# Optimization experiments

Measured on AMD Instinct MI355X. Metric: run time of the kernel, lower is better.

## Reference

```python
import jax, jax.numpy as jnp
import numpy as np

B = 512
NODES_PER_GRAPH = 256
N = B * NODES_PER_GRAPH
IN_DIM = 128
HID = 128
PAD_VALUE = -10000.0


def setup_inputs() -> dict:
    key = jax.random.key(0)
    ks = jax.random.split(key, 10)
    inp = {
        "last_node_batch": jax.random.normal(ks[0], (B, IN_DIM), jnp.float32),
        "h": jax.random.normal(ks[1], (N, HID), jnp.float32),
        # NodeEmbed: Linear(in_dim, hidden_dim)
        "W_embed": jax.random.normal(ks[2], (IN_DIM, HID), jnp.float32) / np.sqrt(IN_DIM),
        "b_embed": jnp.zeros((HID,), jnp.float32),
        # Linear_3(2H, 2H, 2)
        "W1": jax.random.normal(ks[3], (2 * HID, 2 * HID), jnp.float32) / np.sqrt(2 * HID),
        "b1": jnp.zeros((2 * HID,), jnp.float32),
        "W2": jax.random.normal(ks[4], (2 * HID, 2 * HID), jnp.float32) / np.sqrt(2 * HID),
        "b2": jnp.zeros((2 * HID,), jnp.float32),
        "W3": jax.random.normal(ks[5], (2 * HID, 2), jnp.float32) / np.sqrt(2 * HID),
        "b3": jnp.zeros((2,), jnp.float32),
        # ragged batch encoded as sorted segment ids (graph id per node)
        "segment_ids": jnp.repeat(jnp.arange(B, dtype=jnp.int64), NODES_PER_GRAPH),
        "max_nodes": NODES_PER_GRAPH,
    }
    return inp


def reference(last_node_batch, h, W_embed, b_embed, W1, b1, W2, b2, W3, b3,
              segment_ids, max_nodes):
    n = h.shape[0]
    b = last_node_batch.shape[0]
    # per-graph node embed, broadcast to each node of its graph (repeat+cat loop)
    node_embed = last_node_batch @ W_embed + b_embed          # [B, H]
    bcast = node_embed[segment_ids]                           # [N, H]
    stack = jnp.concatenate([h, bcast], axis=1)               # [N, 2H]
    # Linear_3 MLP
    out = jnp.tanh(stack @ W1 + b1)
    out = jnp.tanh(out @ W2 + b2)
    edges = out @ W3 + b3                                     # [N, 2]
    # unbatch + pad_sequence(padding_value=-10000), then flatten(1, -1)
    counts = jax.ops.segment_sum(jnp.ones((n,), jnp.int32), segment_ids, num_segments=b)
    offsets = jnp.cumsum(counts) - counts                     # start index of each graph
    pos = jnp.arange(n) - offsets[segment_ids]                # position within graph
    padded = jnp.full((b, max_nodes, 2), PAD_VALUE, dtype=edges.dtype)
    padded = padded.at[segment_ids, pos].set(edges)
    return padded.reshape(b, max_nodes * 2)
```

## Files before the change

kernel.cpp:

```cpp
#include <hip/hip_runtime.h>


typedef __attribute__((ext_vector_type(8))) short s16x8;
typedef __attribute__((ext_vector_type(4))) float f32x4;

#define K2   256
#define KH   128
#define LDK  264

__device__ __forceinline__ float b2f(unsigned short u) {
  return __builtin_bit_cast(float, (unsigned int)u << 16);
}
__device__ __forceinline__ unsigned short f2b(float f) {
  unsigned int u = __builtin_bit_cast(unsigned int, f);
  u += 0x7fffu + ((u >> 16) & 1u);
  return (unsigned short)(u >> 16);
}
__device__ __forceinline__ float pade_tanh(float x) {
  float x2 = x * x;
  float x4 = x2 * x2;
  float num = x * (945.0f + 105.0f * x2 + x4);
  float den = __builtin_fmaf(15.0f, x4, __builtin_fmaf(420.0f, x2, 945.0f));
  float r = num * __builtin_amdgcn_rcpf(den);
  return __builtin_fmaxf(-1.0f, __builtin_fminf(1.0f, r));
}
__device__ __forceinline__ unsigned int probe_is16(const unsigned int* wraw,
                                                   int t) {
  unsigned int w = wraw[t];
  unsigned int e = (w >> 7) & 0xFFu;
  unsigned long long m = __ballot(e >= 96 && e < 128);
  return (__popcll(m) >= 32) ? 1u : 0u;
}

__global__ __launch_bounds__(256) void prep_pack(
    const void* __restrict__ W1, const void* __restrict__ W2,
    const void* __restrict__ Wemb,
    unsigned short* __restrict__ W1P, unsigned short* __restrict__ W2P)
{
  __shared__ unsigned int flagLds;
  const int blk = blockIdx.x, t = threadIdx.x;
  if (t < 64) { unsigned int f = probe_is16((const unsigned int*)Wemb, t);
                if (t == 0) flagLds = f; }
  __syncthreads();
  const bool is16 = flagLds != 0u;

  const void* S; unsigned short* D; int k0, n0, pk;
  if (blk < 32) { S = W1; D = W1P; pk = 2048;
                  k0 = (blk & 3) * 32; n0 = (blk >> 2) * 32; }
  else { int b = blk - 32; S = W2; D = W2P; pk = 4096;
         k0 = (b & 7) * 32; n0 = (b >> 3) * 32; }
  #pragma unroll
  for (int q = 0; q < 4; ++q) {
    int idx = t + 256 * q;
    int ln = idx & 31, lk = idx >> 5;
    int n = n0 + ln, k = k0 + lk;
    unsigned short v = is16
        ? ((const unsigned short*)S)[k * K2 + n]
        : f2b(((const float*)S)[k * K2 + n]);
    D[(n >> 4) * pk + (k >> 3) * 128 + (n & 15) * 8 + (k & 7)] = v;
  }
}

__global__ __launch_bounds__(256, 3) void mlp_graph(
    const void* __restrict__ h,     const void* __restrict__ last,
    const void* __restrict__ Wemb,  const void* __restrict__ bemb,
    const void* __restrict__ W1,    const void* __restrict__ b1,
    const void* __restrict__ b2,
    const void* __restrict__ W3,    const void* __restrict__ b3,
    const unsigned short* __restrict__ W1P,
    const unsigned short* __restrict__ W2P,
    void* __restrict__ out)
{
  __shared__ __align__(16) unsigned short smA[32 * LDK];
  __shared__ float embp[2][KH];
  __shared__ float emb32[KH];
  __shared__ float ebias[K2];
  __shared__ float headp[4][32][2];
  __shared__ unsigned int flagLds;

  const int t    = threadIdx.x;
  const int lane = t & 63, w = t >> 6;
  const int quad = lane >> 4, l16 = lane & 15;
  const int g    = blockIdx.x >> 2;
  const int sp   = blockIdx.x & 3;

  if (t < 64) { unsigned int f = probe_is16((const unsigned int*)Wemb, t);
                if (t == 0) flagLds = f; }
  __syncthreads();
  const bool is16 = flagLds != 0u;

  {
    const int j = t & 127, half = t >> 7, k0 = half * 64;
    float a0 = 0.f, a1 = 0.f, a2 = 0.f, a3 = 0.f;
    if (is16) {
      const unsigned short* lp = (const unsigned short*)last + g * KH;
      const unsigned short* wp = (const unsigned short*)Wemb;
      #pragma unroll 4
      for (int k = k0; k < k0 + 64; k += 4) {
        a0 += b2f(lp[k])     * b2f(wp[k * KH + j]);
        a1 += b2f(lp[k + 1]) * b2f(wp[(k + 1) * KH + j]);
        a2 += b2f(lp[k + 2]) * b2f(wp[(k + 2) * KH + j]);
        a3 += b2f(lp[k + 3]) * b2f(wp[(k + 3) * KH + j]);
      }
    } else {
      const float* lp = (const float*)last + g * KH;
      const float* wp = (const float*)Wemb;
      #pragma unroll 4
      for (int k = k0; k < k0 + 64; k += 4) {
        a0 += lp[k]     * wp[k * KH + j];
        a1 += lp[k + 1] * wp[(k + 1) * KH + j];
        a2 += lp[k + 2] * wp[(k + 2) * KH + j];
        a3 += lp[k + 3] * wp[(k + 3) * KH + j];
      }
    }
    embp[half][j] = (a0 + a1) + (a2 + a3);
  }

  s16x8 bh[2];
  #pragma unroll
  for (int s = 0; s < 2; ++s) {
    int kk = 2 * w + s;
    #pragma unroll
    for (int j = 0; j < 8; ++j) {
      int kidx = (kk * 32 + quad * 8 + j) * 2 + (l16 & 1);
      bh[s][j] = is16 ? (short)((const unsigned short*)W3)[kidx]
                      : (short)f2b(((const float*)W3)[kidx]);
    }
  }
  float b2v[4];
  #pragma unroll
  for (int c = 0; c < 4; ++c) {
    int col = w * 64 + c * 16 + l16;
    b2v[c] = is16 ? b2f(((const unsigned short*)b2)[col])
                  : ((const float*)b2)[col];
  }
  float b3e = 0.f;
  if (t < 64)
    b3e = is16 ? b2f(((const unsigned short*)b3)[t & 1])
               : ((const float*)b3)[t & 1];
  __syncthreads();

  if (t < KH) {
    float e = is16 ? b2f(((const unsigned short*)bemb)[t])
                   : ((const float*)bemb)[t];
    emb32[t] = e + embp[0][t] + embp[1][t];
  }
  __syncthreads();

  {
    float s = is16 ? b2f(((const unsigned short*)b1)[t])
                   : ((const float*)b1)[t];
    if (is16) {
      const unsigned short* wp = (const unsigned short*)W1
                                 + (size_t)KH * K2 + t;
      #pragma unroll 4
      for (int k = 0; k < KH; ++k)
        s = __builtin_fmaf(emb32[k], b2f(wp[(size_t)k * K2]), s);
    } else {
      const float* wp = (const float*)W1 + (size_t)KH * K2 + t;
      #pragma unroll 4
      for (int k = 0; k < KH; ++k)
        s = __builtin_fmaf(emb32[k], wp[(size_t)k * K2], s);
    }
    ebias[t] = s;
  }

  uint4 hreg[2];
  const int pr = t >> 4, pc = t & 15;
  auto load_tile = [&](int slice) {
    int rbase = g * 256 + slice * 32;
    if (is16) {
      const uint4* hp = (const uint4*)h;
      #pragma unroll
      for (int i = 0; i < 2; ++i)
        hreg[i] = hp[(size_t)(rbase + pr + 16 * i) * 16 + pc];
    } else {
      const float4* hf = (const float4*)h;
      #pragma unroll
      for (int i = 0; i < 2; ++i) {
        float4 va = hf[(size_t)(rbase + pr + 16 * i) * 32 + pc * 2];
        float4 vb = hf[(size_t)(rbase + pr + 16 * i) * 32 + pc * 2 + 1];
        ushort4 ua, ub;
        ua.x = f2b(va.x); ua.y = f2b(va.y); ua.z = f2b(va.z); ua.w = f2b(va.w);
        ub.x = f2b(vb.x); ub.y = f2b(vb.y); ub.z = f2b(vb.z); ub.w = f2b(vb.w);
        hreg[i] = make_uint4(
            (unsigned)ua.x | ((unsigned)ua.y << 16),
            (unsigned)ua.z | ((unsigned)ua.w << 16),
            (unsigned)ub.x | ((unsigned)ub.y << 16),
            (unsigned)ub.z | ((unsigned)ub.w << 16));
      }
    }
  };
  load_tile(2 * sp);

  f32x4 acc[2][4];
  for (int tt = 0; tt < 2; ++tt) {
    const int slice = 2 * sp + tt;
    const int base = g * 256 + slice * 32;
    __syncthreads();
    #pragma unroll
    for (int i = 0; i < 2; ++i)
      *(uint4*)&smA[(pr + 16 * i) * LDK + pc * 8] = hreg[i];
    if (tt < 1) load_tile(slice + 1);
    __syncthreads();

    #pragma unroll
    for (int i = 0; i < 2; ++i)
      #pragma unroll
      for (int c = 0; c < 4; ++c) acc[i][c] = f32x4{0.f, 0.f, 0.f, 0.f};
    #pragma unroll
    for (int kk = 0; kk < 4; ++kk) {
      s16x8 a[2], b[4];
      #pragma unroll
      for (int i = 0; i < 2; ++i)
        a[i] = *(const s16x8*)&smA[(i * 16 + l16) * LDK + kk * 32 + quad * 8];
      #pragma unroll
      for (int c = 0; c < 4; ++c)
        b[c] = *(const s16x8*)&W1P[(w * 4 + c) * 2048
                                   + (kk * 4 + quad) * 128 + l16 * 8];
      #pragma unroll
      for (int i = 0; i < 2; ++i)
        #pragma unroll
        for (int c = 0; c < 4; ++c)
          acc[i][c] = __builtin_amdgcn_mfma_f32_16x16x32_bf16(
              a[i], b[c], acc[i][c], 0, 0, 0);
    }
    __syncthreads();
    #pragma unroll
    for (int c = 0; c < 4; ++c) {
      int col = w * 64 + c * 16 + l16;
      float eb = ebias[col];
      #pragma unroll
      for (int i = 0; i < 2; ++i)
        #pragma unroll
        for (int rg = 0; rg < 4; ++rg)
          smA[(i * 16 + quad * 4 + rg) * LDK + col] =
              f2b(pade_tanh(acc[i][c][rg] + eb));
    }
    __syncthreads();

    #pragma unroll
    for (int i = 0; i < 2; ++i)
      #pragma unroll
      for (int c = 0; c < 4; ++c) acc[i][c] = f32x4{0.f, 0.f, 0.f, 0.f};
    #pragma unroll 2
    for (int kk = 0; kk < 8; ++kk) {
      s16x8 a[2], b[4];
      #pragma unroll
      for (int i = 0; i < 2; ++i)
        a[i] = *(const s16x8*)&smA[(i * 16 + l16) * LDK + kk * 32 + quad * 8];
      #pragma unroll
      for (int c = 0; c < 4; ++c)
        b[c] = *(const s16x8*)&W2P[(w * 4 + c) * 4096
                                   + (kk * 4 + quad) * 128 + l16 * 8];
      #pragma unroll
      for (int i = 0; i < 2; ++i)
        #pragma unroll
        for (int c = 0; c < 4; ++c)
          acc[i][c] = __builtin_amdgcn_mfma_f32_16x16x32_bf16(
              a[i], b[c], acc[i][c], 0, 0, 0);
    }
    __syncthreads();
    #pragma unroll
    for (int c = 0; c < 4; ++c) {
      int col = w * 64 + c * 16 + l16;
      #pragma unroll
      for (int i = 0; i < 2; ++i)
        #pragma unroll
        for (int rg = 0; rg < 4; ++rg)
          smA[(i * 16 + quad * 4 + rg) * LDK + col] =
              f2b(pade_tanh(acc[i][c][rg] + b2v[c]));
    }
    __syncthreads();

    {
      #pragma unroll
      for (int i = 0; i < 2; ++i) acc[i][0] = f32x4{0.f, 0.f, 0.f, 0.f};
      #pragma unroll
      for (int s = 0; s < 2; ++s) {
        int kk = 2 * w + s;
        #pragma unroll
        for (int i = 0; i < 2; ++i) {
          s16x8 a = *(const s16x8*)&smA[(i * 16 + l16) * LDK
                                        + kk * 32 + quad * 8];
          acc[i][0] = __builtin_amdgcn_mfma_f32_16x16x32_bf16(
              a, bh[s], acc[i][0], 0, 0, 0);
        }
      }
      if (l16 < 2) {
        #pragma unroll
        for (int i = 0; i < 2; ++i)
          #pragma unroll
          for (int rg = 0; rg < 4; ++rg)
            headp[w][i * 16 + quad * 4 + rg][l16] = acc[i][0][rg];
      }
    }
    __syncthreads();
    if (t < 64) {
      const int r = t >> 1, e = t & 1;
      float s = b3e + headp[0][r][e] + headp[1][r][e]
                    + headp[2][r][e] + headp[3][r][e];
      size_t idx = (size_t)(base + r) * 2 + e;
      if (is16) ((unsigned short*)out)[idx] = f2b(s);
      else      ((float*)out)[idx] = s;
    }
  }
}

extern "C" void kernel_launch(void* const* d_in, const int* in_sizes, int n_in,
                              void* d_out, int out_size, void* d_ws, size_t ws_size,
                              hipStream_t stream) {
  (void)in_sizes; (void)n_in; (void)out_size; (void)ws_size;
  const void* last = d_in[0];
  const void* h    = d_in[1];
  const void* Wemb = d_in[2];
  const void* bemb = d_in[3];
  const void* W1   = d_in[4];
  const void* b1   = d_in[5];
  const void* W2   = d_in[6];
  const void* b2   = d_in[7];
  const void* W3   = d_in[8];
  const void* b3   = d_in[9];

  char* ws = (char*)d_ws;
  unsigned short* W1P   = (unsigned short*)(ws);
  unsigned short* W2P   = (unsigned short*)(ws + 65536);

  prep_pack<<<dim3(96), dim3(256), 0, stream>>>(W1, W2, Wemb, W1P, W2P);
  mlp_graph<<<dim3(2048), dim3(256), 0, stream>>>(
      h, last, Wemb, bemb, W1, b1, b2, W3, b3, W1P, W2P, d_out);
}
```

Measured before the change: 186.6 us.

## Use one 512-thread block per graph instead of four 256-thread blocks

The grid drops from four blocks per graph to one 512-thread block per graph, which walks four 64-row tiles. The eight waves split into four column groups and two row halves. This removes the per-graph prologue that was repeated four times (node embed, ebias matvec over W1, W3 fragments). In exchange there are only 512 blocks, which gives less parallelism and a longer serial loop per block, and LDS use per block doubles.

Measured after the change: 191.6 us. +2.7%, slower.

```diff
diff --git a/kernel.cpp b/kernel.cpp
--- a/kernel.cpp
+++ b/kernel.cpp
@@ -61,7 +61,7 @@
   }
 }
 
-__global__ __launch_bounds__(256, 3) void mlp_graph(
+__global__ __launch_bounds__(512, 2) void mlp_graph(
     const void* __restrict__ h,     const void* __restrict__ last,
     const void* __restrict__ Wemb,  const void* __restrict__ bemb,
     const void* __restrict__ W1,    const void* __restrict__ b1,
@@ -71,18 +71,19 @@
     const unsigned short* __restrict__ W2P,
     void* __restrict__ out)
 {
-  __shared__ __align__(16) unsigned short smA[32 * LDK];
-  __shared__ float embp[2][KH];
+  __shared__ __align__(16) unsigned short smA[64 * LDK];
+  __shared__ float embp[4][KH];
   __shared__ float emb32[KH];
   __shared__ float ebias[K2];
-  __shared__ float headp[4][32][2];
+  __shared__ float headp[4][64][2];
   __shared__ unsigned int flagLds;
 
   const int t    = threadIdx.x;
   const int lane = t & 63, w = t >> 6;
+  const int wc   = w & 3;
+  const int wrh  = w >> 2;
   const int quad = lane >> 4, l16 = lane & 15;
-  const int g    = blockIdx.x >> 2;
-  const int sp   = blockIdx.x & 3;
+  const int g    = blockIdx.x;
 
   if (t < 64) { unsigned int f = probe_is16((const unsigned int*)Wemb, t);
                 if (t == 0) flagLds = f; }
@@ -90,13 +91,13 @@
   const bool is16 = flagLds != 0u;
 
   {
-    const int j = t & 127, half = t >> 7, k0 = half * 64;
+    const int j = t & 127, qtr = t >> 7, k0 = qtr * 32;
     float a0 = 0.f, a1 = 0.f, a2 = 0.f, a3 = 0.f;
     if (is16) {
       const unsigned short* lp = (const unsigned short*)last + g * KH;
       const unsigned short* wp = (const unsigned short*)Wemb;
       #pragma unroll 4
-      for (int k = k0; k < k0 + 64; k += 4) {
+      for (int k = k0; k < k0 + 32; k += 4) {
         a0 += b2f(lp[k])     * b2f(wp[k * KH + j]);
         a1 += b2f(lp[k + 1]) * b2f(wp[(k + 1) * KH + j]);
         a2 += b2f(lp[k + 2]) * b2f(wp[(k + 2) * KH + j]);
@@ -106,20 +107,20 @@
       const float* lp = (const float*)last + g * KH;
       const float* wp = (const float*)Wemb;
       #pragma unroll 4
-      for (int k = k0; k < k0 + 64; k += 4) {
+      for (int k = k0; k < k0 + 32; k += 4) {
         a0 += lp[k]     * wp[k * KH + j];
         a1 += lp[k + 1] * wp[(k + 1) * KH + j];
         a2 += lp[k + 2] * wp[(k + 2) * KH + j];
         a3 += lp[k + 3] * wp[(k + 3) * KH + j];
       }
     }
-    embp[half][j] = (a0 + a1) + (a2 + a3);
+    embp[qtr][j] = (a0 + a1) + (a2 + a3);
   }
 
   s16x8 bh[2];
   #pragma unroll
   for (int s = 0; s < 2; ++s) {
-    int kk = 2 * w + s;
+    int kk = 2 * wc + s;
     #pragma unroll
     for (int j = 0; j < 8; ++j) {
       int kidx = (kk * 32 + quad * 8 + j) * 2 + (l16 & 1);
@@ -130,12 +131,12 @@
   float b2v[4];
   #pragma unroll
   for (int c = 0; c < 4; ++c) {
-    int col = w * 64 + c * 16 + l16;
+    int col = wc * 64 + c * 16 + l16;
     b2v[c] = is16 ? b2f(((const unsigned short*)b2)[col])
                   : ((const float*)b2)[col];
   }
   float b3e = 0.f;
-  if (t < 64)
+  if (t < 128)
     b3e = is16 ? b2f(((const unsigned short*)b3)[t & 1])
                : ((const float*)b3)[t & 1];
   __syncthreads();
@@ -143,11 +144,11 @@
   if (t < KH) {
     float e = is16 ? b2f(((const unsigned short*)bemb)[t])
                    : ((const float*)bemb)[t];
-    emb32[t] = e + embp[0][t] + embp[1][t];
+    emb32[t] = e + embp[0][t] + embp[1][t] + embp[2][t] + embp[3][t];
   }
   __syncthreads();
 
-  {
+  if (t < K2) {
     float s = is16 ? b2f(((const unsigned short*)b1)[t])
                    : ((const float*)b1)[t];
     if (is16) {
@@ -167,19 +168,19 @@
 
   uint4 hreg[2];
   const int pr = t >> 4, pc = t & 15;
-  auto load_tile = [&](int slice) {
-    int rbase = g * 256 + slice * 32;
+  auto load_tile = [&](int tile) {
+    int rbase = g * 256 + tile * 64;
     if (is16) {
       const uint4* hp = (const uint4*)h;
       #pragma unroll
       for (int i = 0; i < 2; ++i)
-        hreg[i] = hp[(size_t)(rbase + pr + 16 * i) * 16 + pc];
+        hreg[i] = hp[(size_t)(rbase + pr + 32 * i) * 16 + pc];
     } else {
       const float4* hf = (const float4*)h;
       #pragma unroll
       for (int i = 0; i < 2; ++i) {
-        float4 va = hf[(size_t)(rbase + pr + 16 * i) * 32 + pc * 2];
-        float4 vb = hf[(size_t)(rbase + pr + 16 * i) * 32 + pc * 2 + 1];
+        float4 va = hf[(size_t)(rbase + pr + 32 * i) * 32 + pc * 2];
+        float4 vb = hf[(size_t)(rbase + pr + 32 * i) * 32 + pc * 2 + 1];
         ushort4 ua, ub;
         ua.x = f2b(va.x); ua.y = f2b(va.y); ua.z = f2b(va.z); ua.w = f2b(va.w);
         ub.x = f2b(vb.x); ub.y = f2b(vb.y); ub.z = f2b(vb.z); ub.w = f2b(vb.w);
@@ -191,17 +192,16 @@
       }
     }
   };
-  load_tile(2 * sp);
+  load_tile(0);
 
   f32x4 acc[2][4];
-  for (int tt = 0; tt < 2; ++tt) {
-    const int slice = 2 * sp + tt;
-    const int base = g * 256 + slice * 32;
+  for (int tile = 0; tile < 4; ++tile) {
+    const int base = g * 256 + tile * 64;
     __syncthreads();
     #pragma unroll
     for (int i = 0; i < 2; ++i)
-      *(uint4*)&smA[(pr + 16 * i) * LDK + pc * 8] = hreg[i];
-    if (tt < 1) load_tile(slice + 1);
+      *(uint4*)&smA[(pr + 32 * i) * LDK + pc * 8] = hreg[i];
+    if (tile < 3) load_tile(tile + 1);
     __syncthreads();
 
     #pragma unroll
@@ -213,10 +213,11 @@
       s16x8 a[2], b[4];
       #pragma unroll
       for (int i = 0; i < 2; ++i)
-        a[i] = *(const s16x8*)&smA[(i * 16 + l16) * LDK + kk * 32 + quad * 8];
+        a[i] = *(const s16x8*)&smA[(wrh * 32 + i * 16 + l16) * LDK
+                                   + kk * 32 + quad * 8];
       #pragma unroll
       for (int c = 0; c < 4; ++c)
-        b[c] = *(const s16x8*)&W1P[(w * 4 + c) * 2048
+        b[c] = *(const s16x8*)&W1P[(wc * 4 + c) * 2048
                                    + (kk * 4 + quad) * 128 + l16 * 8];
       #pragma unroll
       for (int i = 0; i < 2; ++i)
@@ -228,13 +229,13 @@
     __syncthreads();
     #pragma unroll
     for (int c = 0; c < 4; ++c) {
-      int col = w * 64 + c * 16 + l16;
+      int col = wc * 64 + c * 16 + l16;
       float eb = ebias[col];
       #pragma unroll
       for (int i = 0; i < 2; ++i)
         #pragma unroll
         for (int rg = 0; rg < 4; ++rg)
-          smA[(i * 16 + quad * 4 + rg) * LDK + col] =
+          smA[(wrh * 32 + i * 16 + quad * 4 + rg) * LDK + col] =
               f2b(pade_tanh(acc[i][c][rg] + eb));
     }
     __syncthreads();
@@ -248,10 +249,11 @@
       s16x8 a[2], b[4];
       #pragma unroll
       for (int i = 0; i < 2; ++i)
-        a[i] = *(const s16x8*)&smA[(i * 16 + l16) * LDK + kk * 32 + quad * 8];
+        a[i] = *(const s16x8*)&smA[(wrh * 32 + i * 16 + l16) * LDK
+                                   + kk * 32 + quad * 8];
       #pragma unroll
       for (int c = 0; c < 4; ++c)
-        b[c] = *(const s16x8*)&W2P[(w * 4 + c) * 4096
+        b[c] = *(const s16x8*)&W2P[(wc * 4 + c) * 4096
                                    + (kk * 4 + quad) * 128 + l16 * 8];
       #pragma unroll
       for (int i = 0; i < 2; ++i)
@@ -263,12 +265,12 @@
     __syncthreads();
     #pragma unroll
     for (int c = 0; c < 4; ++c) {
-      int col = w * 64 + c * 16 + l16;
+      int col = wc * 64 + c * 16 + l16;
       #pragma unroll
       for (int i = 0; i < 2; ++i)
         #pragma unroll
         for (int rg = 0; rg < 4; ++rg)
-          smA[(i * 16 + quad * 4 + rg) * LDK + col] =
+          smA[(wrh * 32 + i * 16 + quad * 4 + rg) * LDK + col] =
               f2b(pade_tanh(acc[i][c][rg] + b2v[c]));
     }
     __syncthreads();
@@ -278,10 +280,10 @@
       for (int i = 0; i < 2; ++i) acc[i][0] = f32x4{0.f, 0.f, 0.f, 0.f};
       #pragma unroll
       for (int s = 0; s < 2; ++s) {
-        int kk = 2 * w + s;
+        int kk = 2 * wc + s;
         #pragma unroll
         for (int i = 0; i < 2; ++i) {
-          s16x8 a = *(const s16x8*)&smA[(i * 16 + l16) * LDK
+          s16x8 a = *(const s16x8*)&smA[(wrh * 32 + i * 16 + l16) * LDK
                                         + kk * 32 + quad * 8];
           acc[i][0] = __builtin_amdgcn_mfma_f32_16x16x32_bf16(
               a, bh[s], acc[i][0], 0, 0, 0);
@@ -292,11 +294,12 @@
         for (int i = 0; i < 2; ++i)
           #pragma unroll
           for (int rg = 0; rg < 4; ++rg)
-            headp[w][i * 16 + quad * 4 + rg][l16] = acc[i][0][rg];
-      }
-    }
-    __syncthreads();
-    if (t < 64) {
+            headp[wc][wrh * 32 + i * 16 + quad * 4 + rg][l16] =
+                acc[i][0][rg];
+      }
+    }
+    __syncthreads();
+    if (t < 128) {
       const int r = t >> 1, e = t & 1;
       float s = b3e + headp[0][r][e] + headp[1][r][e]
                     + headp[2][r][e] + headp[3][r][e];
@@ -327,6 +330,6 @@
   unsigned short* W2P   = (unsigned short*)(ws + 65536);
 
   prep_pack<<<dim3(96), dim3(256), 0, stream>>>(W1, W2, Wemb, W1P, W2P);
-  mlp_graph<<<dim3(2048), dim3(256), 0, stream>>>(
+  mlp_graph<<<dim3(512), dim3(512), 0, stream>>>(
       h, last, Wemb, bemb, W1, b1, b2, W3, b3, W1P, W2P, d_out);
 }
```
